# Optimization experiments

Measured on AMD Instinct MI355X. Metric: run time of the kernel, lower is better.

## Reference

```python
import jax, jax.numpy as jnp
import numpy as np

N_T, D_MODEL, RANK, BATCH = 64, 1024, 8, 4096
THRESHOLD = 0.0  # jumprelu threshold (forward default)


def setup_inputs() -> dict:
    key = jax.random.key(0)
    k_x, k_v, k_u, k_e = jax.random.split(key, 4)
    scale = (1.0 / (D_MODEL * RANK)) ** 0.25
    x = jax.random.normal(k_x, (BATCH, D_MODEL), dtype=jnp.float32)
    V = jax.random.normal(k_v, (N_T, RANK, D_MODEL), dtype=jnp.float32) * scale
    U = jax.random.normal(k_u, (N_T, D_MODEL, RANK), dtype=jnp.float32) * scale
    encoder = jax.random.normal(k_e, (N_T, D_MODEL), dtype=jnp.float32)
    encoder = encoder / jnp.linalg.norm(encoder, axis=1, keepdims=True)
    bias = -jnp.ones((N_T,), dtype=jnp.float32)  # init_constant(bias, -1.0)
    return {"x": x, "V": V, "U": U, "encoder": encoder, "bias": bias}


def jumprelu(x, threshold=THRESHOLD):
    # forward: hard threshold x * 1[x > threshold]
    return x * (x > threshold).astype(x.dtype)


def reference(x, V, U, encoder, bias):
    # pre_acts: (batch, n)
    pre_acts = x @ encoder.T - bias
    gate = jumprelu(pre_acts)  # activation_fn='jumprelu', threshold=0.0
    # Vx: (n, batch, rank)
    Vx = jnp.einsum('nrd,bd->nbr', V, x)
    # UVx: (n, batch, d) -- the large intermediate a fused kernel would avoid
    UVx = jnp.einsum('ndr,nbr->nbd', U, Vx)
    # gated sum over transforms: (batch, d)
    output = jnp.einsum('nbd,bn->bd', UVx, gate)
    u_norms = jnp.linalg.norm(U.reshape(U.shape[0], -1), axis=1)
    v_norms = jnp.linalg.norm(V.reshape(V.shape[0], -1), axis=1)
    frobenius_norms = u_norms * v_norms / (D_MODEL * RANK) ** 0.5
    return output, gate, frobenius_norms
```

## Files before the change

kernel.cpp:

```cpp
#include <hip/hip_runtime.h>
#include <math.h>

#define BATCHN 4096
#define DMODEL 1024
#define NT 64
#define RANK 8
#define K2 512

typedef __attribute__((ext_vector_type(8))) short bf16x8;
typedef __attribute__((ext_vector_type(4))) float f32x4;

__device__ __forceinline__ void async16(void* lds, const void* g) {
    __builtin_amdgcn_global_load_lds(
        (const __attribute__((address_space(1))) void*)g,
        (__attribute__((address_space(3))) void*)lds, 16, 0, 0);
}

__device__ __forceinline__ short f2bf(float f) {
    unsigned u = __builtin_bit_cast(unsigned, f);
    u += 0x7fffu + ((u >> 16) & 1u);
    return (short)(u >> 16);
}

__global__ __launch_bounds__(256) void convert_kernel(
    const float* __restrict__ x, const float* __restrict__ enc,
    const float* __restrict__ V, const float* __restrict__ U,
    unsigned short* __restrict__ xb, unsigned short* __restrict__ Wb,
    unsigned short* __restrict__ Ub,
    float* __restrict__ su_part, float* __restrict__ sv_part)
{
    const int b = blockIdx.x, t = threadIdx.x;
    const float* src;
    unsigned short* dst;
    float* psum = nullptr;
    if (b < 2048) {
        const int e0 = b * 2048 + t * 8;
        src = x + e0; dst = xb + e0;
    } else if (b < 2336) {
        const int e0 = (b - 2048) * 2048 + t * 8;
        const int row = e0 >> 10, col = e0 & 1023;
        if (row < 64) {
            src = enc + (size_t)row * 1024 + col;
        } else {
            src = V + (size_t)(row - 64) * 1024 + col;
            const int vrow = (b - 2048) * 2 - 64;
            psum = sv_part + (vrow >> 3) * 4 + ((vrow & 7) >> 1);
        }
        dst = Wb + e0;
    } else {
        const int bi = b - 2336;
        const int e0 = bi * 2048 + t * 8;
        src = U + e0; dst = Ub + e0;
        psum = su_part + (bi >> 2) * 4 + (bi & 3);
    }
    float4 v0 = *(const float4*)src;
    float4 v1 = *(const float4*)(src + 4);
    bf16x8 o;
    o[0] = f2bf(v0.x); o[1] = f2bf(v0.y); o[2] = f2bf(v0.z); o[3] = f2bf(v0.w);
    o[4] = f2bf(v1.x); o[5] = f2bf(v1.y); o[6] = f2bf(v1.z); o[7] = f2bf(v1.w);
    *(bf16x8*)dst = o;

    if (psum) {
        float s = v0.x*v0.x + v0.y*v0.y + v0.z*v0.z + v0.w*v0.w
                + v1.x*v1.x + v1.y*v1.y + v1.z*v1.z + v1.w*v1.w;
        #pragma unroll
        for (int off = 32; off; off >>= 1) s += __shfl_down(s, off);
        __shared__ float red[4];
        if ((t & 63) == 0) red[t >> 6] = s;
        __syncthreads();
        if (t == 0) *psum = red[0] + red[1] + red[2] + red[3];
    }
}

__global__ __launch_bounds__(256) void gatevx_kernel(
    const unsigned short* __restrict__ A, const unsigned short* __restrict__ Bm,
    const float* __restrict__ bias,
    float* __restrict__ gate_out, unsigned short* __restrict__ vx_out)
{
    constexpr int BK = 64, KDIM = DMODEL, NIT = KDIM / BK;
    __shared__ unsigned short As[2][64 * BK];
    __shared__ unsigned short Bs[2][64 * BK];
    const int t = threadIdx.x;
    const int wave = t >> 6, lane = t & 63;
    const int bm = blockIdx.y, bn = blockIdx.x;
    const int wm = wave & 1, wn = wave >> 1;
    const int lrow = lane >> 3, lchunk = lane & 7;
    const int l15 = lane & 15, lq = lane >> 4;

    f32x4 acc[2][2] = {};
    const size_t Abase = (size_t)bm * 64 * KDIM;
    const size_t Bbase = (size_t)bn * 64 * KDIM;

    auto STAGE = [&](int buf, int k0) {
        #pragma unroll
        for (int c = 0; c < 2; ++c) {
            const int row = (wave * 2 + c) * 8 + lrow;
            const int chunk = lchunk ^ lrow;
            async16(&As[buf][(wave * 2 + c) * 512],
                    A + Abase + (size_t)row * KDIM + k0 + chunk * 8);
            async16(&Bs[buf][(wave * 2 + c) * 512],
                    Bm + Bbase + (size_t)row * KDIM + k0 + chunk * 8);
        }
    };
    auto COMPUTE = [&](int buf) {
        #pragma unroll
        for (int s = 0; s < 2; ++s) {
            bf16x8 af[2], bfr[2];
            const int kc = s * 4 + lq;
            #pragma unroll
            for (int i = 0; i < 2; ++i) {
                const int m = wm * 32 + i * 16 + l15;
                af[i] = *(const bf16x8*)&As[buf][m * BK + ((kc ^ (m & 7)) * 8)];
            }
            #pragma unroll
            for (int j = 0; j < 2; ++j) {
                const int n = wn * 32 + j * 16 + l15;
                bfr[j] = *(const bf16x8*)&Bs[buf][n * BK + ((kc ^ (n & 7)) * 8)];
            }
            #pragma unroll
            for (int i = 0; i < 2; ++i)
                #pragma unroll
                for (int j = 0; j < 2; ++j)
                    acc[i][j] = __builtin_amdgcn_mfma_f32_16x16x32_bf16(
                        af[i], bfr[j], acc[i][j], 0, 0, 0);
        }
    };

    STAGE(0, 0);
    __syncthreads();
    int cur = 0;
    for (int kt = 0; kt < NIT - 1; ++kt) {
        STAGE(cur ^ 1, (kt + 1) * BK);
        COMPUTE(cur);
        __syncthreads();
        cur ^= 1;
    }
    COMPUTE(cur);

    #pragma unroll
    for (int i = 0; i < 2; ++i) {
        const int rowb = bm * 64 + wm * 32 + i * 16 + lq * 4;
        #pragma unroll
        for (int j = 0; j < 2; ++j) {
            const int col = wn * 32 + j * 16 + l15;
            #pragma unroll
            for (int r = 0; r < 4; ++r) {
                const int row = rowb + r;
                const float v = acc[i][j][r];
                if (bn == 0) {
                    const float p = v - bias[col];
                    gate_out[(size_t)row * NT + col] = p > 0.f ? p : 0.f;
                } else {
                    vx_out[(size_t)row * K2 + (bn - 1) * 64 + col] = (unsigned short)f2bf(v);
                }
            }
        }
    }
}

__global__ __launch_bounds__(256) void out_kernel(
    const unsigned short* __restrict__ vx, const float* __restrict__ gate,
    const unsigned short* __restrict__ Ub, float* __restrict__ out,
    const float* __restrict__ su_part, const float* __restrict__ sv_part,
    float* __restrict__ fro)
{
    constexpr int BK = 64, KDIM = K2, NIT = KDIM / BK;
    __shared__ unsigned short As[2][64 * BK];
    __shared__ unsigned short Bs[2][8 * 2 * 64 * 8];
    const int t = threadIdx.x;
    const int wave = t >> 6, lane = t & 63;
    const int bm = blockIdx.y, bn = blockIdx.x;
    const int wm = wave & 1, wn = wave >> 1;
    const int lrow = lane >> 3, lchunk = lane & 7;
    const int l15 = lane & 15, lq = lane >> 4;

    f32x4 acc[2][4] = {};

    auto LOADA = [&](int k0, bf16x8* v, float* g) {
        #pragma unroll
        for (int c = 0; c < 2; ++c) {
            const int row = (wave * 2 + c) * 8 + lrow;
            const int grow = bm * 64 + row;
            const int chunk = lchunk ^ lrow;
            v[c] = *(const bf16x8*)(vx + (size_t)grow * K2 + k0 + chunk * 8);
            g[c] = gate[(size_t)grow * NT + (k0 >> 3) + chunk];
        }
    };
    auto WRITEA = [&](int buf, const bf16x8* v, const float* g) {
        #pragma unroll
        for (int c = 0; c < 2; ++c) {
            bf16x8 o;
            #pragma unroll
            for (int e = 0; e < 8; ++e) {
                const float f = __builtin_bit_cast(float,
                    ((unsigned)(unsigned short)v[c][e]) << 16);
                o[e] = (short)(__builtin_bit_cast(unsigned, f * g[c]) >> 16);
            }
            *(bf16x8*)&As[buf][(wave * 2 + c) * 512 + lane * 8] = o;
        }
    };
    auto STAGEB = [&](int buf, int k0) {
        #pragma unroll
        for (int c = 0; c < 4; ++c) {
            const int n_local = wave * 2 + (c >> 1);
            const int dblk = c & 1;
            const int n_glob = (k0 >> 3) + n_local;
            async16(&Bs[buf][(n_local * 2 + dblk) * 512],
                    Ub + (size_t)n_glob * (DMODEL * RANK)
                       + (size_t)(bn * 128 + dblk * 64 + lane) * RANK);
        }
    };
    auto COMPUTE = [&](int buf) {
        #pragma unroll
        for (int s = 0; s < 2; ++s) {
            bf16x8 af[2], bfr[4];
            const int kc = s * 4 + lq;
            #pragma unroll
            for (int i = 0; i < 2; ++i) {
                const int m = wm * 32 + i * 16 + l15;
                af[i] = *(const bf16x8*)&As[buf][m * BK + ((kc ^ (m & 7)) * 8)];
            }
            #pragma unroll
            for (int j = 0; j < 4; ++j) {
                const int cl = wn * 64 + j * 16 + l15;
                bfr[j] = *(const bf16x8*)&Bs[buf][((kc * 2 + (cl >> 6)) * 64 + (cl & 63)) * 8];
            }
            #pragma unroll
            for (int i = 0; i < 2; ++i)
                #pragma unroll
                for (int j = 0; j < 4; ++j)
                    acc[i][j] = __builtin_amdgcn_mfma_f32_16x16x32_bf16(
                        af[i], bfr[j], acc[i][j], 0, 0, 0);
        }
    };

    {
        bf16x8 v[2]; float g[2];
        LOADA(0, v, g);
        STAGEB(0, 0);
        WRITEA(0, v, g);
    }
    __syncthreads();
    int cur = 0;
    for (int kt = 0; kt < NIT - 1; ++kt) {
        bf16x8 v[2]; float g[2];
        LOADA((kt + 1) * BK, v, g);
        STAGEB(cur ^ 1, (kt + 1) * BK);
        COMPUTE(cur);
        WRITEA(cur ^ 1, v, g);
        __syncthreads();
        cur ^= 1;
    }
    COMPUTE(cur);

    #pragma unroll
    for (int i = 0; i < 2; ++i) {
        const int rowb = bm * 64 + wm * 32 + i * 16 + lq * 4;
        #pragma unroll
        for (int j = 0; j < 4; ++j) {
            const int col = bn * 128 + wn * 64 + j * 16 + l15;
            #pragma unroll
            for (int r = 0; r < 4; ++r)
                out[(size_t)(rowb + r) * DMODEL + col] = acc[i][j][r];
        }
    }

    if (bn == 0 && bm == 0 && t < NT) {
        float su = su_part[t * 4] + su_part[t * 4 + 1] + su_part[t * 4 + 2] + su_part[t * 4 + 3];
        float sv = sv_part[t * 4] + sv_part[t * 4 + 1] + sv_part[t * 4 + 2] + sv_part[t * 4 + 3];
        fro[t] = sqrtf(su) * sqrtf(sv) / sqrtf((float)(DMODEL * RANK));
    }
}

extern "C" void kernel_launch(void* const* d_in, const int* in_sizes, int n_in,
                              void* d_out, int out_size, void* d_ws, size_t ws_size,
                              hipStream_t stream) {
    const float* x    = (const float*)d_in[0];
    const float* V    = (const float*)d_in[1];
    const float* U    = (const float*)d_in[2];
    const float* enc  = (const float*)d_in[3];
    const float* bias = (const float*)d_in[4];

    float* out  = (float*)d_out;
    float* gate = out + (size_t)BATCHN * DMODEL;
    float* fro  = gate + (size_t)BATCHN * NT;

    char* ws = (char*)d_ws;
    unsigned short* xb = (unsigned short*)ws;
    unsigned short* Wb = (unsigned short*)(ws + 8388608);
    unsigned short* Ub = (unsigned short*)(ws + 9568256);
    unsigned short* vx = (unsigned short*)(ws + 10616832);
    float* su_part     = (float*)(ws + 14811136);
    float* sv_part     = (float*)(ws + 14812160);

    convert_kernel<<<2592, 256, 0, stream>>>(x, enc, V, U, xb, Wb, Ub, su_part, sv_part);
    gatevx_kernel<<<dim3(9, 64), 256, 0, stream>>>(xb, Wb, bias, gate, vx);
    out_kernel<<<dim3(8, 64), 256, 0, stream>>>(vx, gate, Ub, out, su_part, sv_part, fro);
}
```

Baseline: 109.8 us.

## Stage GEMM epilogues through LDS for vector stores; coarsen convert blocks

The convert kernel now gives each block four 2048-element chunks, so one block covers a whole transform's norm partial and there is no multi-part reduction. Both GEMM epilogues first write their accumulators into the freed LDS buffers, then issue coalesced 16-byte vector stores instead of scattered scalar stores. This is meant to cut store transactions and launch or block overhead. The cost is extra barriers and an LDS round trip in each epilogue.

```diff
diff --git a/kernel.cpp b/kernel.cpp
--- a/kernel.cpp
+++ b/kernel.cpp
@@ -30,39 +30,61 @@
     float* __restrict__ su_part, float* __restrict__ sv_part)
 {
     const int b = blockIdx.x, t = threadIdx.x;
-    const float* src;
-    unsigned short* dst;
+    float s = 0.f;
     float* psum = nullptr;
-    if (b < 2048) {
-        const int e0 = b * 2048 + t * 8;
-        src = x + e0; dst = xb + e0;
-    } else if (b < 2336) {
-        const int e0 = (b - 2048) * 2048 + t * 8;
-        const int row = e0 >> 10, col = e0 & 1023;
-        if (row < 64) {
-            src = enc + (size_t)row * 1024 + col;
-        } else {
-            src = V + (size_t)(row - 64) * 1024 + col;
-            const int vrow = (b - 2048) * 2 - 64;
-            psum = sv_part + (vrow >> 3) * 4 + ((vrow & 7) >> 1);
-        }
-        dst = Wb + e0;
+
+    if (b < 512) {
+        const size_t base = (size_t)b * 8192;
+        #pragma unroll
+        for (int it = 0; it < 4; ++it) {
+            const size_t e = base + it * 2048 + t * 8;
+            float4 v0 = *(const float4*)(x + e);
+            float4 v1 = *(const float4*)(x + e + 4);
+            bf16x8 o;
+            o[0]=f2bf(v0.x); o[1]=f2bf(v0.y); o[2]=f2bf(v0.z); o[3]=f2bf(v0.w);
+            o[4]=f2bf(v1.x); o[5]=f2bf(v1.y); o[6]=f2bf(v1.z); o[7]=f2bf(v1.w);
+            *(bf16x8*)(xb + e) = o;
+        }
+    } else if (b < 584) {
+        const size_t base = (size_t)(b - 512) * 8192;
+        const bool isV = (b >= 520);
+        if (isV) psum = sv_part + (b - 520);
+        #pragma unroll
+        for (int it = 0; it < 4; ++it) {
+            const size_t e = base + it * 2048 + t * 8;
+            const int row = (int)(e >> 10), col = (int)(e & 1023);
+            const float* src = (row < 64)
+                ? enc + (size_t)row * 1024 + col
+                : V + (size_t)(row - 64) * 1024 + col;
+            float4 v0 = *(const float4*)src;
+            float4 v1 = *(const float4*)(src + 4);
+            bf16x8 o;
+            o[0]=f2bf(v0.x); o[1]=f2bf(v0.y); o[2]=f2bf(v0.z); o[3]=f2bf(v0.w);
+            o[4]=f2bf(v1.x); o[5]=f2bf(v1.y); o[6]=f2bf(v1.z); o[7]=f2bf(v1.w);
+            *(bf16x8*)(Wb + e) = o;
+            if (isV)
+                s += v0.x*v0.x + v0.y*v0.y + v0.z*v0.z + v0.w*v0.w
+                   + v1.x*v1.x + v1.y*v1.y + v1.z*v1.z + v1.w*v1.w;
+        }
     } else {
-        const int bi = b - 2336;
-        const int e0 = bi * 2048 + t * 8;
-        src = U + e0; dst = Ub + e0;
-        psum = su_part + (bi >> 2) * 4 + (bi & 3);
-    }
-    float4 v0 = *(const float4*)src;
-    float4 v1 = *(const float4*)(src + 4);
-    bf16x8 o;
-    o[0] = f2bf(v0.x); o[1] = f2bf(v0.y); o[2] = f2bf(v0.z); o[3] = f2bf(v0.w);
-    o[4] = f2bf(v1.x); o[5] = f2bf(v1.y); o[6] = f2bf(v1.z); o[7] = f2bf(v1.w);
-    *(bf16x8*)dst = o;
+        const int n = b - 584;
+        psum = su_part + n;
+        const size_t base = (size_t)n * 8192;
+        #pragma unroll
+        for (int it = 0; it < 4; ++it) {
+            const size_t e = base + it * 2048 + t * 8;
+            float4 v0 = *(const float4*)(U + e);
+            float4 v1 = *(const float4*)(U + e + 4);
+            bf16x8 o;
+            o[0]=f2bf(v0.x); o[1]=f2bf(v0.y); o[2]=f2bf(v0.z); o[3]=f2bf(v0.w);
+            o[4]=f2bf(v1.x); o[5]=f2bf(v1.y); o[6]=f2bf(v1.z); o[7]=f2bf(v1.w);
+            *(bf16x8*)(Ub + e) = o;
+            s += v0.x*v0.x + v0.y*v0.y + v0.z*v0.z + v0.w*v0.w
+               + v1.x*v1.x + v1.y*v1.y + v1.z*v1.z + v1.w*v1.w;
+        }
+    }
 
     if (psum) {
-        float s = v0.x*v0.x + v0.y*v0.y + v0.z*v0.z + v0.w*v0.w
-                + v1.x*v1.x + v1.y*v1.y + v1.z*v1.z + v1.w*v1.w;
         #pragma unroll
         for (int off = 32; off; off >>= 1) s += __shfl_down(s, off);
         __shared__ float red[4];
@@ -136,24 +158,52 @@
         cur ^= 1;
     }
     COMPUTE(cur);
-
-    #pragma unroll
-    for (int i = 0; i < 2; ++i) {
-        const int rowb = bm * 64 + wm * 32 + i * 16 + lq * 4;
-        #pragma unroll
-        for (int j = 0; j < 2; ++j) {
-            const int col = wn * 32 + j * 16 + l15;
-            #pragma unroll
-            for (int r = 0; r < 4; ++r) {
-                const int row = rowb + r;
-                const float v = acc[i][j][r];
-                if (bn == 0) {
-                    const float p = v - bias[col];
-                    gate_out[(size_t)row * NT + col] = p > 0.f ? p : 0.f;
-                } else {
-                    vx_out[(size_t)row * K2 + (bn - 1) * 64 + col] = (unsigned short)f2bf(v);
+    __syncthreads();
+
+    if (bn == 0) {
+        float* Cs = (float*)&As[0][0];
+        #pragma unroll
+        for (int i = 0; i < 2; ++i) {
+            const int rowb = wm * 32 + i * 16 + lq * 4;
+            #pragma unroll
+            for (int j = 0; j < 2; ++j) {
+                const int col = wn * 32 + j * 16 + l15;
+                const float bz = bias[col];
+                #pragma unroll
+                for (int r = 0; r < 4; ++r) {
+                    const float p = acc[i][j][r] - bz;
+                    Cs[(rowb + r) * 64 + col] = p > 0.f ? p : 0.f;
                 }
             }
+        }
+        __syncthreads();
+        #pragma unroll
+        for (int p = 0; p < 4; ++p) {
+            const int row = p * 16 + (t >> 4);
+            const int col = (t & 15) * 4;
+            *(f32x4*)&gate_out[(size_t)(bm * 64 + row) * NT + col] =
+                *(const f32x4*)&Cs[row * 64 + col];
+        }
+    } else {
+        unsigned short* Cs16 = &As[0][0];
+        #pragma unroll
+        for (int i = 0; i < 2; ++i) {
+            const int rowb = wm * 32 + i * 16 + lq * 4;
+            #pragma unroll
+            for (int j = 0; j < 2; ++j) {
+                const int col = wn * 32 + j * 16 + l15;
+                #pragma unroll
+                for (int r = 0; r < 4; ++r)
+                    Cs16[(rowb + r) * 64 + col] = (unsigned short)f2bf(acc[i][j][r]);
+            }
+        }
+        __syncthreads();
+        #pragma unroll
+        for (int p = 0; p < 2; ++p) {
+            const int row = p * 32 + (t >> 3);
+            const int chunk = t & 7;
+            *(bf16x8*)&vx_out[(size_t)(bm * 64 + row) * K2 + (bn - 1) * 64 + chunk * 8] =
+                *(const bf16x8*)&Cs16[row * 64 + chunk * 8];
         }
     }
 }
@@ -252,23 +302,31 @@
         cur ^= 1;
     }
     COMPUTE(cur);
-
+    __syncthreads();
+
+    float* Cs = (float*)&Bs[0][0];
     #pragma unroll
     for (int i = 0; i < 2; ++i) {
-        const int rowb = bm * 64 + wm * 32 + i * 16 + lq * 4;
+        const int rowb = wm * 32 + i * 16 + lq * 4;
         #pragma unroll
         for (int j = 0; j < 4; ++j) {
-            const int col = bn * 128 + wn * 64 + j * 16 + l15;
+            const int col = wn * 64 + j * 16 + l15;
             #pragma unroll
             for (int r = 0; r < 4; ++r)
-                out[(size_t)(rowb + r) * DMODEL + col] = acc[i][j][r];
-        }
+                Cs[(rowb + r) * 128 + col] = acc[i][j][r];
+        }
+    }
+    __syncthreads();
+    #pragma unroll
+    for (int p = 0; p < 8; ++p) {
+        const int row = p * 8 + (t >> 5);
+        const int col = (t & 31) * 4;
+        *(f32x4*)&out[(size_t)(bm * 64 + row) * DMODEL + bn * 128 + col] =
+            *(const f32x4*)&Cs[row * 128 + col];
     }
 
     if (bn == 0 && bm == 0 && t < NT) {
-        float su = su_part[t * 4] + su_part[t * 4 + 1] + su_part[t * 4 + 2] + su_part[t * 4 + 3];
-        float sv = sv_part[t * 4] + sv_part[t * 4 + 1] + sv_part[t * 4 + 2] + sv_part[t * 4 + 3];
-        fro[t] = sqrtf(su) * sqrtf(sv) / sqrtf((float)(DMODEL * RANK));
+        fro[t] = sqrtf(su_part[t]) * sqrtf(sv_part[t]) / sqrtf((float)(DMODEL * RANK));
     }
 }
 
@@ -293,7 +351,7 @@
     float* su_part     = (float*)(ws + 14811136);
     float* sv_part     = (float*)(ws + 14812160);
 
-    convert_kernel<<<2592, 256, 0, stream>>>(x, enc, V, U, xb, Wb, Ub, su_part, sv_part);
+    convert_kernel<<<648, 256, 0, stream>>>(x, enc, V, U, xb, Wb, Ub, su_part, sv_part);
     gatevx_kernel<<<dim3(9, 64), 256, 0, stream>>>(xb, Wb, bias, gate, vx);
     out_kernel<<<dim3(8, 64), 256, 0, stream>>>(vx, gate, Ub, out, su_part, sv_part, fro);
 }
```

Result: no change. 110.4 us (+0.6%).
